# Kernel optimization log

Measured on AMD Instinct MI355X. Metric: run time of the kernel, lower is better.

## Reference

```python
import jax, jax.numpy as jnp
import numpy as np

T, N, E = 48, 1000, 32000
D_IN, H = 32, 64


def setup_inputs() -> dict:
    key = jax.random.key(0)
    ks = jax.random.split(key, 14)
    p = lambda k, s: (jax.random.normal(k, s, dtype=jnp.float32) * 0.05)
    return {
        "x": jax.random.normal(ks[0], (T, N, D_IN), dtype=jnp.float32),
        "edge_index": jax.random.randint(ks[1], (2, E), 0, N, dtype=jnp.int32),
        "hidden_state": jnp.zeros((N, H), jnp.float32),
        "cell_state": jnp.zeros((N, H), jnp.float32),
        # GCNConv 1 (lin weight stored as [in, out] so x @ W matches x @ lin.weight.T)
        "Wg1": p(ks[2], (D_IN, H)), "bg1": p(ks[3], (H,)),
        # GCNConv 2
        "Wg2": p(ks[4], (H, H)), "bg2": p(ks[5], (H,)),
        # LSTMCell params, torch gate order (i, f, g, o)
        "W_ih": p(ks[6], (4 * H, H)), "W_hh": p(ks[7], (4 * H, H)),
        "b_ih": p(ks[8], (4 * H,)), "b_hh": p(ks[9], (4 * H,)),
        # final Linear(hidden_dim * num_nodes -> num_nodes)
        "W_lin": p(ks[10], (N, H * N)), "b_lin": p(ks[11], (N,)),
    }


def _gcn_norm(edge_index, num_nodes):
    """PyG GCNConv default: add self loops, symmetric D^-1/2 (A+I) D^-1/2 norm."""
    loops = jnp.arange(num_nodes, dtype=edge_index.dtype)
    src = jnp.concatenate([edge_index[0], loops])
    dst = jnp.concatenate([edge_index[1], loops])
    deg = jax.ops.segment_sum(jnp.ones(src.shape[0], jnp.float32), dst,
                              num_segments=num_nodes)
    dinv = jax.lax.rsqrt(jnp.maximum(deg, 1.0))  # self loops guarantee deg >= 1
    norm = dinv[src] * dinv[dst]
    return src, dst, norm


def _gcn(x, W, b, src, dst, norm, num_nodes):
    x = x @ W                              # [N, out]
    msg = x[src] * norm[:, None]           # gather + scale  [E+N, out]
    return jax.ops.segment_sum(msg, dst, num_segments=num_nodes) + b


def reference(x, edge_index, hidden_state, cell_state,
              Wg1, bg1, Wg2, bg2, W_ih, W_hh, b_ih, b_hh, W_lin, b_lin):
    src, dst, norm = _gcn_norm(edge_index, N)

    def step(carry, xt):
        h, c = carry
        g = jax.nn.relu(_gcn(xt, Wg1, bg1, src, dst, norm, N))
        g = _gcn(g, Wg2, bg2, src, dst, norm, N)
        gates = g @ W_ih.T + b_ih + h @ W_hh.T + b_hh   # [N, 4H]
        i, f, gg, o = jnp.split(gates, 4, axis=-1)
        c = jax.nn.sigmoid(f) * c + jax.nn.sigmoid(i) * jnp.tanh(gg)
        h = jax.nn.sigmoid(o) * jnp.tanh(c)
        return (h, c), h

    (hidden_state, cell_state), h_seq = jax.lax.scan(step, (hidden_state, cell_state), x)
    flat = h_seq.reshape(T, N * H)                      # view(-1, hidden*num_nodes)
    out = flat @ W_lin.T + b_lin                        # [T, N]
    out = out.reshape(-1, N, 4)                         # [T/4, N, 4]
    return out, hidden_state, cell_state
```

## Files before the change

kernel.cpp:

```cpp
#include <hip/hip_runtime.h>
#include <math.h>

#define T_STEPS 48
#define N_NODES 1000
#define E_EDGES 32000
#define DIN     32
#define H_DIM   64

#define O_INDEG  0
#define O_FILL   1024
#define O_ROWPTR 2048
#define O_CSRC   4096
#define O_CNORM  36864
#define O_DINV   69632
#define O_SELF   70656
#define O_BUF0   71680
#define O_BUF1   (71680 + 3072000)

typedef __attribute__((ext_vector_type(8))) short short8;
typedef __attribute__((ext_vector_type(4))) float f32x4;

__device__ __forceinline__ float sigmf(float v) { return 1.0f / (1.0f + __expf(-v)); }

__global__ void k_zero(int* __restrict__ p) { p[blockIdx.x * 256 + threadIdx.x] = 0; }

__global__ void k_count(const int* __restrict__ ei, int* __restrict__ indeg) {
  int e = blockIdx.x * 256 + threadIdx.x;
  if (e < E_EDGES) atomicAdd(&indeg[ei[E_EDGES + e]], 1);
}

__global__ void k_scan(const int* __restrict__ indeg, int* __restrict__ rowptr,
                       float* __restrict__ dinv, float* __restrict__ selfn) {
  __shared__ int sdat[1024];
  int tid = threadIdx.x;
  int v = (tid < N_NODES) ? indeg[tid] : 0;
  sdat[tid] = v;
  __syncthreads();
  for (int off = 1; off < 1024; off <<= 1) {
    int add = (tid >= off) ? sdat[tid - off] : 0;
    __syncthreads();
    sdat[tid] += add;
    __syncthreads();
  }
  if (tid < N_NODES) {
    rowptr[tid + 1] = sdat[tid];
    float di = rsqrtf((float)(v + 1));
    dinv[tid] = di;
    selfn[tid] = di * di;
  }
  if (tid == 0) rowptr[0] = 0;
}

__global__ void k_scatter(const int* __restrict__ ei, const int* __restrict__ rowptr,
                          int* __restrict__ fill, const float* __restrict__ dinv,
                          int* __restrict__ csrc, float* __restrict__ cnorm) {
  int e = blockIdx.x * 256 + threadIdx.x;
  if (e >= E_EDGES) return;
  int s = ei[e], d = ei[E_EDGES + e];
  int pos = atomicAdd(&fill[d], 1);
  int idx = rowptr[d] + pos;
  csrc[idx] = s;
  cnorm[idx] = dinv[s] * dinv[d];
}

__global__ void __launch_bounds__(256) k_t1(const float* __restrict__ x,
                                            const float* __restrict__ Wg1,
                                            float* __restrict__ T1) {
  __shared__ float sWT[H_DIM * 36];
  __shared__ float sx[4][DIN];
  const int tid = threadIdx.x, wv = tid >> 6, h = tid & 63;
  for (int i = tid; i < DIN * H_DIM; i += 256) sWT[(i & 63) * 36 + (i >> 6)] = Wg1[i];
  __syncthreads();
  const int r0 = blockIdx.x * 64 + wv * 16;
  const float4* wrow = (const float4*)&sWT[h * 36];
  for (int it = 0; it < 16; ++it) {
    const int r = r0 + it;
    if (h < DIN) sx[wv][h] = x[r * DIN + h];
    float acc = 0.f;
    const float4* xp = (const float4*)&sx[wv][0];
#pragma unroll
    for (int k4 = 0; k4 < 8; ++k4) {
      float4 xv = xp[k4], wv4 = wrow[k4];
      acc += xv.x * wv4.x + xv.y * wv4.y + xv.z * wv4.z + xv.w * wv4.w;
    }
    T1[r * H_DIM + h] = acc;
  }
}

__device__ __forceinline__ float gath_node(const float* __restrict__ Tsrc,
                                           const int* __restrict__ es,
                                           const float* __restrict__ ew,
                                           int cnt, int h) {
  float a0 = 0.f, a1 = 0.f, a2 = 0.f, a3 = 0.f;
  float a4 = 0.f, a5 = 0.f, a6 = 0.f, a7 = 0.f;
  int e = 0;
  if (cnt >= 8) {
    float p0 = Tsrc[es[0] * 64 + h], p1 = Tsrc[es[1] * 64 + h];
    float p2 = Tsrc[es[2] * 64 + h], p3 = Tsrc[es[3] * 64 + h];
    float p4 = Tsrc[es[4] * 64 + h], p5 = Tsrc[es[5] * 64 + h];
    float p6 = Tsrc[es[6] * 64 + h], p7 = Tsrc[es[7] * 64 + h];
    for (e = 8; e + 8 <= cnt; e += 8) {
      float n0 = Tsrc[es[e + 0] * 64 + h], n1 = Tsrc[es[e + 1] * 64 + h];
      float n2 = Tsrc[es[e + 2] * 64 + h], n3 = Tsrc[es[e + 3] * 64 + h];
      float n4 = Tsrc[es[e + 4] * 64 + h], n5 = Tsrc[es[e + 5] * 64 + h];
      float n6 = Tsrc[es[e + 6] * 64 + h], n7 = Tsrc[es[e + 7] * 64 + h];
      a0 += ew[e - 8] * p0; a1 += ew[e - 7] * p1;
      a2 += ew[e - 6] * p2; a3 += ew[e - 5] * p3;
      a4 += ew[e - 4] * p4; a5 += ew[e - 3] * p5;
      a6 += ew[e - 2] * p6; a7 += ew[e - 1] * p7;
      p0 = n0; p1 = n1; p2 = n2; p3 = n3; p4 = n4; p5 = n5; p6 = n6; p7 = n7;
    }
    a0 += ew[e - 8] * p0; a1 += ew[e - 7] * p1;
    a2 += ew[e - 6] * p2; a3 += ew[e - 5] * p3;
    a4 += ew[e - 4] * p4; a5 += ew[e - 3] * p5;
    a6 += ew[e - 2] * p6; a7 += ew[e - 1] * p7;
  }
  for (; e < cnt; ++e) a0 += ew[e] * Tsrc[es[e] * 64 + h];
  return ((a0 + a1) + (a2 + a3)) + ((a4 + a5) + (a6 + a7));
}

#define ECHUNK 768
__global__ void __launch_bounds__(256) k_gath(const float* __restrict__ Tall,
                                              const float* __restrict__ bias,
                                              const int* __restrict__ rowptr,
                                              const int* __restrict__ csrc,
                                              const float* __restrict__ cnorm,
                                              const float* __restrict__ selfn,
                                              float* __restrict__ Dall, int relu) {
  __shared__ int   s_src[ECHUNK];
  __shared__ float s_wt[ECHUNK];
  __shared__ float sb[64];
  const int tid = threadIdx.x, wv = tid >> 6, h = tid & 63;
  if (tid < 64) sb[tid] = bias[tid];
  const int t = blockIdx.x >> 6, nb16 = (blockIdx.x & 63) * 16;
  if (nb16 >= N_NODES) return;
  const float* Tsrc = Tall + t * 64000;
  float* dst = Dall + t * 64000;
  const int nE = (nb16 + 16 < N_NODES) ? nb16 + 16 : N_NODES;
  const int r0 = rowptr[nb16], r1 = rowptr[nE];
  const int tot = r1 - r0;
  const bool fits = (tot <= ECHUNK);
  if (fits)
    for (int i = tid; i < tot; i += 256) { s_src[i] = csrc[r0 + i]; s_wt[i] = cnorm[r0 + i]; }
  __syncthreads();
  for (int i = 0; i < 4; ++i) {
    const int n = nb16 + wv * 4 + i;
    if (n >= N_NODES) continue;
    const int a = rowptr[n], b = rowptr[n + 1];
    float acc = selfn[n] * Tsrc[n * 64 + h];
    if (fits) {
      acc += gath_node(Tsrc, s_src + (a - r0), s_wt + (a - r0), b - a, h);
    } else {
      for (int e = a; e < b; ++e) acc += cnorm[e] * Tsrc[csrc[e] * 64 + h];
    }
    acc += sb[h];
    if (relu) acc = fmaxf(acc, 0.f);
    dst[n * 64 + h] = acc;
  }
}

__global__ void __launch_bounds__(256) k_mm2(const float* __restrict__ G1,
                                             const float* __restrict__ Wg2,
                                             float* __restrict__ T2) {
  __shared__ float sW[H_DIM * H_DIM];
  __shared__ float sx[4][H_DIM];
  const int tid = threadIdx.x, wv = tid >> 6, h = tid & 63;
  for (int i = tid; i < H_DIM * H_DIM; i += 256) sW[i] = Wg2[i];
  __syncthreads();
  const int r0 = blockIdx.x * 64 + wv * 16;
  for (int it = 0; it < 16; ++it) {
    const int r = r0 + it;
    sx[wv][h] = G1[r * 64 + h];
    float acc = 0.f;
#pragma unroll
    for (int k = 0; k < H_DIM; ++k) acc += sx[wv][k] * sW[k * H_DIM + h];
    T2[r * 64 + h] = acc;
  }
}

__global__ void __launch_bounds__(256) k_lstm(const float* __restrict__ G2,
                                              const float* __restrict__ h0,
                                              const float* __restrict__ c0,
                                              const float* __restrict__ Wih,
                                              const float* __restrict__ Whh,
                                              const float* __restrict__ bih,
                                              const float* __restrict__ bhh,
                                              float* __restrict__ hsg,
                                              float* __restrict__ outp) {
  const int tid = threadIdx.x, nb = blockIdx.x;
  __shared__ float sh[64];
  __shared__ float sg2[2][64];
  __shared__ float sgates[256];
  float4 Wih4[16], Whh4[16];
  {
    const float4* wp = (const float4*)(Wih + tid * H_DIM);
    const float4* vp = (const float4*)(Whh + tid * H_DIM);
#pragma unroll
    for (int k = 0; k < 16; ++k) { Wih4[k] = wp[k]; Whh4[k] = vp[k]; }
  }
  const float bsum = bih[tid] + bhh[tid];
  float creg = 0.f;
  if (tid < 64) {
    sh[tid] = h0[nb * 64 + tid];
    creg = c0[nb * 64 + tid];
    sg2[0][tid] = G2[nb * 64 + tid];
  }
  __syncthreads();
  for (int t = 0; t < T_STEPS; ++t) {
    const int cur = t & 1;
    float gnext = 0.f;
    if (t < T_STEPS - 1 && tid < 64) gnext = G2[(t + 1) * 64000 + nb * 64 + tid];
    float gv = bsum;
    const float4* gp = (const float4*)&sg2[cur][0];
    const float4* hp = (const float4*)sh;
#pragma unroll
    for (int k = 0; k < 16; ++k) {
      float4 a = gp[k], b = hp[k];
      gv += a.x * Wih4[k].x + a.y * Wih4[k].y + a.z * Wih4[k].z + a.w * Wih4[k].w;
      gv += b.x * Whh4[k].x + b.y * Whh4[k].y + b.z * Whh4[k].z + b.w * Whh4[k].w;
    }
    sgates[tid] = gv;
    __syncthreads();
    if (tid < 64) {
      float iv = sgates[tid], fv = sgates[64 + tid], gg = sgates[128 + tid], ov = sgates[192 + tid];
      float cn = sigmf(fv) * creg + sigmf(iv) * tanhf(gg);
      float hn = sigmf(ov) * tanhf(cn);
      creg = cn;
      sh[tid] = hn;
      hsg[t * 64000 + nb * 64 + tid] = hn;
      if (t < T_STEPS - 1) sg2[cur ^ 1][tid] = gnext;
    }
    __syncthreads();
  }
  if (tid < 64) {
    outp[48000 + nb * 64 + tid] = sh[tid];
    outp[48000 + 64000 + nb * 64 + tid] = creg;
  }
}

__global__ void k_cvt(const float* __restrict__ src, unsigned* __restrict__ dst) {
  const int id = blockIdx.x * 256 + threadIdx.x;
  const float4 v = ((const float4*)src)[id];
  unsigned lo, hi;
  asm("v_cvt_pk_bf16_f32 %0, %1, %2" : "=v"(lo) : "v"(v.x), "v"(v.y));
  asm("v_cvt_pk_bf16_f32 %0, %1, %2" : "=v"(hi) : "v"(v.z), "v"(v.w));
  ((uint2*)dst)[id] = make_uint2(lo, hi);
}

__global__ void __launch_bounds__(256) k_gemmM(const unsigned short* __restrict__ hsb,
                                               const float* __restrict__ Wlin,
                                               float* __restrict__ part) {
  const int tid = threadIdx.x;
  const int kc = blockIdx.x & 15, nt = blockIdx.x >> 4;
  const int wv = tid >> 6, l = tid & 63;
  const int lr = l & 15, kg = l >> 4;
  const int kcbase = kc * 4000;
  const int kp = kc * 4 + wv;

  const unsigned short* ap0 = hsb + (size_t)(0  + lr) * 64000 + kcbase + kg * 8 + wv * 32;
  const unsigned short* ap1 = hsb + (size_t)(16 + lr) * 64000 + kcbase + kg * 8 + wv * 32;
  const unsigned short* ap2 = hsb + (size_t)(32 + lr) * 64000 + kcbase + kg * 8 + wv * 32;
  int nrow = nt * 16 + lr; if (nrow > N_NODES - 1) nrow = N_NODES - 1;
  const float* bp = Wlin + (size_t)nrow * 64000 + kcbase + kg * 8 + wv * 32;

  f32x4 acc0 = {0.f, 0.f, 0.f, 0.f}, acc1 = acc0, acc2 = acc0;

  for (int s = wv; s < 125; s += 4) {
    const short8 a0 = *(const short8*)ap0;
    const short8 a1 = *(const short8*)ap1;
    const short8 a2 = *(const short8*)ap2;
    const float4 b0 = *(const float4*)bp;
    const float4 b1 = *(const float4*)(bp + 4);
    unsigned p0, p1, p2, p3;
    asm("v_cvt_pk_bf16_f32 %0, %1, %2" : "=v"(p0) : "v"(b0.x), "v"(b0.y));
    asm("v_cvt_pk_bf16_f32 %0, %1, %2" : "=v"(p1) : "v"(b0.z), "v"(b0.w));
    asm("v_cvt_pk_bf16_f32 %0, %1, %2" : "=v"(p2) : "v"(b1.x), "v"(b1.y));
    asm("v_cvt_pk_bf16_f32 %0, %1, %2" : "=v"(p3) : "v"(b1.z), "v"(b1.w));
    union { unsigned u[4]; short8 s; } bu;
    bu.u[0] = p0; bu.u[1] = p1; bu.u[2] = p2; bu.u[3] = p3;
    acc0 = __builtin_amdgcn_mfma_f32_16x16x32_bf16(a0, bu.s, acc0, 0, 0, 0);
    acc1 = __builtin_amdgcn_mfma_f32_16x16x32_bf16(a1, bu.s, acc1, 0, 0, 0);
    acc2 = __builtin_amdgcn_mfma_f32_16x16x32_bf16(a2, bu.s, acc2, 0, 0, 0);
    ap0 += 128; ap1 += 128; ap2 += 128; bp += 128;
  }

  const int n = nt * 16 + lr;
  if (n < N_NODES) {
    const int trow = kg * 4;
    float* base = part + (size_t)(kp * 48) * 1000 + n;
#pragma unroll
    for (int j = 0; j < 4; ++j) base[(0  + trow + j) * 1000] = acc0[j];
#pragma unroll
    for (int j = 0; j < 4; ++j) base[(16 + trow + j) * 1000] = acc1[j];
#pragma unroll
    for (int j = 0; j < 4; ++j) base[(32 + trow + j) * 1000] = acc2[j];
  }
}

__global__ void k_reduce(const float* __restrict__ part, const float* __restrict__ blin,
                         float* __restrict__ outp) {
  const int id = blockIdx.x * 256 + threadIdx.x;
  if (id >= T_STEPS * N_NODES) return;
  const int t = id / N_NODES, n = id - t * N_NODES;
  float s = blin[n];
#pragma unroll 8
  for (int kp = 0; kp < 64; ++kp) s += part[(size_t)(kp * 48 + t) * 1000 + n];
  outp[id] = s;
}

extern "C" void kernel_launch(void* const* d_in, const int* in_sizes, int n_in,
                              void* d_out, int out_size, void* d_ws, size_t ws_size,
                              hipStream_t stream) {
  const float* x    = (const float*)d_in[0];
  const int*   ei   = (const int*)d_in[1];
  const float* h0   = (const float*)d_in[2];
  const float* c0   = (const float*)d_in[3];
  const float* Wg1  = (const float*)d_in[4];
  const float* bg1  = (const float*)d_in[5];
  const float* Wg2  = (const float*)d_in[6];
  const float* bg2  = (const float*)d_in[7];
  const float* Wih  = (const float*)d_in[8];
  const float* Whh  = (const float*)d_in[9];
  const float* bih  = (const float*)d_in[10];
  const float* bhh  = (const float*)d_in[11];
  const float* Wlin = (const float*)d_in[12];
  const float* blin = (const float*)d_in[13];
  float* outp = (float*)d_out;
  float* wsf  = (float*)d_ws;
  int*   wsi  = (int*)d_ws;

  int*   indeg  = wsi + O_INDEG;
  int*   fill   = wsi + O_FILL;
  int*   rowptr = wsi + O_ROWPTR;
  int*   csrc   = wsi + O_CSRC;
  float* cnorm  = wsf + O_CNORM;
  float* dinv   = wsf + O_DINV;
  float* selfn  = wsf + O_SELF;
  float* buf0   = wsf + O_BUF0;
  float* buf1   = wsf + O_BUF1;

  k_zero<<<8, 256, 0, stream>>>(wsi);
  k_count<<<(E_EDGES + 255) / 256, 256, 0, stream>>>(ei, indeg);
  k_scan<<<1, 1024, 0, stream>>>(indeg, rowptr, dinv, selfn);
  k_scatter<<<(E_EDGES + 255) / 256, 256, 0, stream>>>(ei, rowptr, fill, dinv, csrc, cnorm);

  k_t1<<<750, 256, 0, stream>>>(x, Wg1, buf0);
  k_gath<<<3072, 256, 0, stream>>>(buf0, bg1, rowptr, csrc, cnorm, selfn, buf1, 1);
  k_mm2<<<750, 256, 0, stream>>>(buf1, Wg2, buf0);
  k_gath<<<3072, 256, 0, stream>>>(buf0, bg2, rowptr, csrc, cnorm, selfn, buf1, 0);
  k_lstm<<<1000, 256, 0, stream>>>(buf1, h0, c0, Wih, Whh, bih, bhh, buf0, outp);

  k_cvt<<<3000, 256, 0, stream>>>(buf0, (unsigned*)buf1);
  k_gemmM<<<16 * 63, 256, 0, stream>>>((const unsigned short*)buf1, Wlin, buf0);
  k_reduce<<<(T_STEPS * N_NODES + 255) / 256, 256, 0, stream>>>(buf0, blin, outp);
}
```

Baseline: 356.3 us.

## Vectorize GCN gather, fuse bf16 conversion into LSTM, prefetch GEMM operands

The gather kernel now splits each node's edges across four lane groups, with each lane loading a float4 of features, and combines the partial sums with cross-lane shuffles. When the workspace is large enough, the LSTM kernel writes hidden states directly as rounded bf16. This removes the separate conversion kernel and one fp32 round trip through memory. The final MFMA GEMM loop also software-prefetches the next A/B fragments to overlap loads with compute. The costs are extra registers and a code path that depends on workspace size.

New measurement: 366.7 us. +2.9%, slower.

```diff
diff --git a/kernel.cpp b/kernel.cpp
--- a/kernel.cpp
+++ b/kernel.cpp
@@ -16,9 +16,12 @@
 #define O_SELF   70656
 #define O_BUF0   71680
 #define O_BUF1   (71680 + 3072000)
+#define O_HSB    (71680 + 6144000)
+#define WS_NEED_HSB ((size_t)(O_HSB + 1536000) * 4)
 
 typedef __attribute__((ext_vector_type(8))) short short8;
 typedef __attribute__((ext_vector_type(4))) float f32x4;
+typedef __attribute__((ext_vector_type(4))) unsigned int uint32x4;
 
 __device__ __forceinline__ float sigmf(float v) { return 1.0f / (1.0f + __expf(-v)); }
 
@@ -87,38 +90,6 @@
   }
 }
 
-__device__ __forceinline__ float gath_node(const float* __restrict__ Tsrc,
-                                           const int* __restrict__ es,
-                                           const float* __restrict__ ew,
-                                           int cnt, int h) {
-  float a0 = 0.f, a1 = 0.f, a2 = 0.f, a3 = 0.f;
-  float a4 = 0.f, a5 = 0.f, a6 = 0.f, a7 = 0.f;
-  int e = 0;
-  if (cnt >= 8) {
-    float p0 = Tsrc[es[0] * 64 + h], p1 = Tsrc[es[1] * 64 + h];
-    float p2 = Tsrc[es[2] * 64 + h], p3 = Tsrc[es[3] * 64 + h];
-    float p4 = Tsrc[es[4] * 64 + h], p5 = Tsrc[es[5] * 64 + h];
-    float p6 = Tsrc[es[6] * 64 + h], p7 = Tsrc[es[7] * 64 + h];
-    for (e = 8; e + 8 <= cnt; e += 8) {
-      float n0 = Tsrc[es[e + 0] * 64 + h], n1 = Tsrc[es[e + 1] * 64 + h];
-      float n2 = Tsrc[es[e + 2] * 64 + h], n3 = Tsrc[es[e + 3] * 64 + h];
-      float n4 = Tsrc[es[e + 4] * 64 + h], n5 = Tsrc[es[e + 5] * 64 + h];
-      float n6 = Tsrc[es[e + 6] * 64 + h], n7 = Tsrc[es[e + 7] * 64 + h];
-      a0 += ew[e - 8] * p0; a1 += ew[e - 7] * p1;
-      a2 += ew[e - 6] * p2; a3 += ew[e - 5] * p3;
-      a4 += ew[e - 4] * p4; a5 += ew[e - 3] * p5;
-      a6 += ew[e - 2] * p6; a7 += ew[e - 1] * p7;
-      p0 = n0; p1 = n1; p2 = n2; p3 = n3; p4 = n4; p5 = n5; p6 = n6; p7 = n7;
-    }
-    a0 += ew[e - 8] * p0; a1 += ew[e - 7] * p1;
-    a2 += ew[e - 6] * p2; a3 += ew[e - 5] * p3;
-    a4 += ew[e - 4] * p4; a5 += ew[e - 3] * p5;
-    a6 += ew[e - 2] * p6; a7 += ew[e - 1] * p7;
-  }
-  for (; e < cnt; ++e) a0 += ew[e] * Tsrc[es[e] * 64 + h];
-  return ((a0 + a1) + (a2 + a3)) + ((a4 + a5) + (a6 + a7));
-}
-
 #define ECHUNK 768
 __global__ void __launch_bounds__(256) k_gath(const float* __restrict__ Tall,
                                               const float* __restrict__ bias,
@@ -129,9 +100,8 @@
                                               float* __restrict__ Dall, int relu) {
   __shared__ int   s_src[ECHUNK];
   __shared__ float s_wt[ECHUNK];
-  __shared__ float sb[64];
-  const int tid = threadIdx.x, wv = tid >> 6, h = tid & 63;
-  if (tid < 64) sb[tid] = bias[tid];
+  const int tid = threadIdx.x, wv = tid >> 6, lane = tid & 63;
+  const int h4 = lane & 15, eq = lane >> 4;
   const int t = blockIdx.x >> 6, nb16 = (blockIdx.x & 63) * 16;
   if (nb16 >= N_NODES) return;
   const float* Tsrc = Tall + t * 64000;
@@ -146,16 +116,58 @@
   for (int i = 0; i < 4; ++i) {
     const int n = nb16 + wv * 4 + i;
     if (n >= N_NODES) continue;
-    const int a = rowptr[n], b = rowptr[n + 1];
-    float acc = selfn[n] * Tsrc[n * 64 + h];
+    const int a = rowptr[n] - r0;
+    const int cnt = rowptr[n] - r0 >= 0 ? rowptr[n + 1] - rowptr[n] : 0;
+    float4 acc = make_float4(0.f, 0.f, 0.f, 0.f);
+    if (eq == 0) {
+      const float4 sv = *(const float4*)&Tsrc[n * 64 + h4 * 4];
+      const float sw = selfn[n];
+      acc.x = sw * sv.x; acc.y = sw * sv.y; acc.z = sw * sv.z; acc.w = sw * sv.w;
+    }
     if (fits) {
-      acc += gath_node(Tsrc, s_src + (a - r0), s_wt + (a - r0), b - a, h);
+      int e = a + eq;
+      const int end = a + cnt;
+      float4 pv = make_float4(0.f, 0.f, 0.f, 0.f);
+      float pw = 0.f;
+      bool have = (e < end);
+      if (have) {
+        const int s = s_src[e]; pw = s_wt[e];
+        pv = *(const float4*)&Tsrc[s * 64 + h4 * 4];
+      }
+      e += 4;
+      while (__any(have)) {
+        float4 nv = make_float4(0.f, 0.f, 0.f, 0.f);
+        float nw = 0.f;
+        const bool hnx = (e < end);
+        if (hnx) {
+          const int s2 = s_src[e]; nw = s_wt[e];
+          nv = *(const float4*)&Tsrc[s2 * 64 + h4 * 4];
+        }
+        acc.x += pw * pv.x; acc.y += pw * pv.y; acc.z += pw * pv.z; acc.w += pw * pv.w;
+        pv = nv; pw = nw; have = hnx; e += 4;
+      }
     } else {
-      for (int e = a; e < b; ++e) acc += cnorm[e] * Tsrc[csrc[e] * 64 + h];
-    }
-    acc += sb[h];
-    if (relu) acc = fmaxf(acc, 0.f);
-    dst[n * 64 + h] = acc;
+      const int A = rowptr[n], B = rowptr[n + 1];
+      for (int e2 = A + eq; e2 < B; e2 += 4) {
+        const int s = csrc[e2];
+        const float w = cnorm[e2];
+        const float4 v = *(const float4*)&Tsrc[s * 64 + h4 * 4];
+        acc.x += w * v.x; acc.y += w * v.y; acc.z += w * v.z; acc.w += w * v.w;
+      }
+    }
+    acc.x += __shfl_xor(acc.x, 16, 64); acc.y += __shfl_xor(acc.y, 16, 64);
+    acc.z += __shfl_xor(acc.z, 16, 64); acc.w += __shfl_xor(acc.w, 16, 64);
+    acc.x += __shfl_xor(acc.x, 32, 64); acc.y += __shfl_xor(acc.y, 32, 64);
+    acc.z += __shfl_xor(acc.z, 32, 64); acc.w += __shfl_xor(acc.w, 32, 64);
+    if (eq == 0) {
+      const float4 b4 = *(const float4*)&bias[h4 * 4];
+      float4 o = make_float4(acc.x + b4.x, acc.y + b4.y, acc.z + b4.z, acc.w + b4.w);
+      if (relu) {
+        o.x = fmaxf(o.x, 0.f); o.y = fmaxf(o.y, 0.f);
+        o.z = fmaxf(o.z, 0.f); o.w = fmaxf(o.w, 0.f);
+      }
+      *(float4*)&dst[n * 64 + h4 * 4] = o;
+    }
   }
 }
 
@@ -186,6 +198,7 @@
                                               const float* __restrict__ bih,
                                               const float* __restrict__ bhh,
                                               float* __restrict__ hsg,
+                                              unsigned short* __restrict__ hsb,
                                               float* __restrict__ outp) {
   const int tid = threadIdx.x, nb = blockIdx.x;
   __shared__ float sh[64];
@@ -227,7 +240,13 @@
       float hn = sigmf(ov) * tanhf(cn);
       creg = cn;
       sh[tid] = hn;
-      hsg[t * 64000 + nb * 64 + tid] = hn;
+      if (hsb) {
+        unsigned u = __float_as_uint(hn);
+        u += 0x7fff + ((u >> 16) & 1);
+        hsb[t * 64000 + nb * 64 + tid] = (unsigned short)(u >> 16);
+      } else {
+        hsg[t * 64000 + nb * 64 + tid] = hn;
+      }
       if (t < T_STEPS - 1) sg2[cur ^ 1][tid] = gnext;
     }
     __syncthreads();
@@ -265,23 +284,33 @@
 
   f32x4 acc0 = {0.f, 0.f, 0.f, 0.f}, acc1 = acc0, acc2 = acc0;
 
+  short8 a0c = *(const short8*)ap0;
+  short8 a1c = *(const short8*)ap1;
+  short8 a2c = *(const short8*)ap2;
+  float4 b0c = *(const float4*)bp;
+  float4 b1c = *(const float4*)(bp + 4);
+
   for (int s = wv; s < 125; s += 4) {
-    const short8 a0 = *(const short8*)ap0;
-    const short8 a1 = *(const short8*)ap1;
-    const short8 a2 = *(const short8*)ap2;
-    const float4 b0 = *(const float4*)bp;
-    const float4 b1 = *(const float4*)(bp + 4);
+    short8 a0n, a1n, a2n; float4 b0n, b1n;
+    if (s + 4 < 125) {
+      ap0 += 128; ap1 += 128; ap2 += 128; bp += 128;
+      a0n = *(const short8*)ap0;
+      a1n = *(const short8*)ap1;
+      a2n = *(const short8*)ap2;
+      b0n = *(const float4*)bp;
+      b1n = *(const float4*)(bp + 4);
+    }
     unsigned p0, p1, p2, p3;
-    asm("v_cvt_pk_bf16_f32 %0, %1, %2" : "=v"(p0) : "v"(b0.x), "v"(b0.y));
-    asm("v_cvt_pk_bf16_f32 %0, %1, %2" : "=v"(p1) : "v"(b0.z), "v"(b0.w));
-    asm("v_cvt_pk_bf16_f32 %0, %1, %2" : "=v"(p2) : "v"(b1.x), "v"(b1.y));
-    asm("v_cvt_pk_bf16_f32 %0, %1, %2" : "=v"(p3) : "v"(b1.z), "v"(b1.w));
-    union { unsigned u[4]; short8 s; } bu;
-    bu.u[0] = p0; bu.u[1] = p1; bu.u[2] = p2; bu.u[3] = p3;
-    acc0 = __builtin_amdgcn_mfma_f32_16x16x32_bf16(a0, bu.s, acc0, 0, 0, 0);
-    acc1 = __builtin_amdgcn_mfma_f32_16x16x32_bf16(a1, bu.s, acc1, 0, 0, 0);
-    acc2 = __builtin_amdgcn_mfma_f32_16x16x32_bf16(a2, bu.s, acc2, 0, 0, 0);
-    ap0 += 128; ap1 += 128; ap2 += 128; bp += 128;
+    asm("v_cvt_pk_bf16_f32 %0, %1, %2" : "=v"(p0) : "v"(b0c.x), "v"(b0c.y));
+    asm("v_cvt_pk_bf16_f32 %0, %1, %2" : "=v"(p1) : "v"(b0c.z), "v"(b0c.w));
+    asm("v_cvt_pk_bf16_f32 %0, %1, %2" : "=v"(p2) : "v"(b1c.x), "v"(b1c.y));
+    asm("v_cvt_pk_bf16_f32 %0, %1, %2" : "=v"(p3) : "v"(b1c.z), "v"(b1c.w));
+    uint32x4 bu = {p0, p1, p2, p3};
+    const short8 bs = __builtin_bit_cast(short8, bu);
+    acc0 = __builtin_amdgcn_mfma_f32_16x16x32_bf16(a0c, bs, acc0, 0, 0, 0);
+    acc1 = __builtin_amdgcn_mfma_f32_16x16x32_bf16(a1c, bs, acc1, 0, 0, 0);
+    acc2 = __builtin_amdgcn_mfma_f32_16x16x32_bf16(a2c, bs, acc2, 0, 0, 0);
+    a0c = a0n; a1c = a1n; a2c = a2n; b0c = b0n; b1c = b1n;
   }
 
   const int n = nt * 16 + lr;
@@ -339,6 +368,8 @@
   float* buf0   = wsf + O_BUF0;
   float* buf1   = wsf + O_BUF1;
 
+  const bool big = ws_size >= WS_NEED_HSB;
+
   k_zero<<<8, 256, 0, stream>>>(wsi);
   k_count<<<(E_EDGES + 255) / 256, 256, 0, stream>>>(ei, indeg);
   k_scan<<<1, 1024, 0, stream>>>(indeg, rowptr, dinv, selfn);
@@ -348,9 +379,18 @@
   k_gath<<<3072, 256, 0, stream>>>(buf0, bg1, rowptr, csrc, cnorm, selfn, buf1, 1);
   k_mm2<<<750, 256, 0, stream>>>(buf1, Wg2, buf0);
   k_gath<<<3072, 256, 0, stream>>>(buf0, bg2, rowptr, csrc, cnorm, selfn, buf1, 0);
-  k_lstm<<<1000, 256, 0, stream>>>(buf1, h0, c0, Wih, Whh, bih, bhh, buf0, outp);
-
-  k_cvt<<<3000, 256, 0, stream>>>(buf0, (unsigned*)buf1);
-  k_gemmM<<<16 * 63, 256, 0, stream>>>((const unsigned short*)buf1, Wlin, buf0);
+
+  unsigned short* hsb;
+  if (big) {
+    hsb = (unsigned short*)(wsf + O_HSB);
+    k_lstm<<<1000, 256, 0, stream>>>(buf1, h0, c0, Wih, Whh, bih, bhh,
+                                     buf0, hsb, outp);
+  } else {
+    k_lstm<<<1000, 256, 0, stream>>>(buf1, h0, c0, Wih, Whh, bih, bhh,
+                                     buf0, (unsigned short*)nullptr, outp);
+    k_cvt<<<3000, 256, 0, stream>>>(buf0, (unsigned*)buf1);
+    hsb = (unsigned short*)buf1;
+  }
+  k_gemmM<<<16 * 63, 256, 0, stream>>>(hsb, Wlin, buf0);
   k_reduce<<<(T_STEPS * N_NODES + 255) / 256, 256, 0, stream>>>(buf0, blin, outp);
 }
```

## Fuse bf16 hidden-state conversion into LSTM and pipeline final GEMM through LDS

Applied to the files above, without the earlier changes.

The LSTM kernel now writes its hidden states directly as bf16 into a new workspace region, which removes the separate conversion kernel. The final linear layer gets a new GEMM kernel that triple-buffers hidden-state and W_lin tiles in LDS using async global_load_lds with swizzled addressing. The K split changes from 64 to 100 partials. This path is chosen only when the workspace is large enough, and it adds more partial sums for the reduce kernel to read.

Measured after the change: 368.9 us. 3.5% more time.

```diff
diff --git a/kernel.cpp b/kernel.cpp
--- a/kernel.cpp
+++ b/kernel.cpp
@@ -16,11 +16,19 @@
 #define O_SELF   70656
 #define O_BUF0   71680
 #define O_BUF1   (71680 + 3072000)
+#define O_HSB    (71680 + 6144000)
+#define WS_NEED_HSB ((size_t)(O_HSB + 1536000) * 4)
 
 typedef __attribute__((ext_vector_type(8))) short short8;
 typedef __attribute__((ext_vector_type(4))) float f32x4;
+typedef __attribute__((ext_vector_type(4))) unsigned int uint32x4;
 
 __device__ __forceinline__ float sigmf(float v) { return 1.0f / (1.0f + __expf(-v)); }
+
+__device__ __forceinline__ void gld16(const void* g, void* l) {
+  __builtin_amdgcn_global_load_lds((const __attribute__((address_space(1))) void*)g,
+                                   (__attribute__((address_space(3))) void*)l, 16, 0, 0);
+}
 
 __global__ void k_zero(int* __restrict__ p) { p[blockIdx.x * 256 + threadIdx.x] = 0; }
 
@@ -186,6 +194,7 @@
                                               const float* __restrict__ bih,
                                               const float* __restrict__ bhh,
                                               float* __restrict__ hsg,
+                                              unsigned short* __restrict__ hsb,
                                               float* __restrict__ outp) {
   const int tid = threadIdx.x, nb = blockIdx.x;
   __shared__ float sh[64];
@@ -227,7 +236,13 @@
       float hn = sigmf(ov) * tanhf(cn);
       creg = cn;
       sh[tid] = hn;
-      hsg[t * 64000 + nb * 64 + tid] = hn;
+      if (hsb) {
+        unsigned u = __float_as_uint(hn);
+        u += 0x7fff + ((u >> 16) & 1);
+        hsb[t * 64000 + nb * 64 + tid] = (unsigned short)(u >> 16);
+      } else {
+        hsg[t * 64000 + nb * 64 + tid] = hn;
+      }
       if (t < T_STEPS - 1) sg2[cur ^ 1][tid] = gnext;
     }
     __syncthreads();
@@ -245,6 +260,104 @@
   asm("v_cvt_pk_bf16_f32 %0, %1, %2" : "=v"(lo) : "v"(v.x), "v"(v.y));
   asm("v_cvt_pk_bf16_f32 %0, %1, %2" : "=v"(hi) : "v"(v.z), "v"(v.w));
   ((uint2*)dst)[id] = make_uint2(lo, hi);
+}
+
+#define G16_KC   25
+#define G16_KR   2560
+#define G16_NCH  20
+#define G16_AF   3072
+#define G16_BF   5120
+
+__global__ void __launch_bounds__(256) k_gemm16(const unsigned short* __restrict__ hsb,
+                                                const float* __restrict__ Wlin,
+                                                float* __restrict__ part) {
+  __shared__ float lds[3 * G16_BF];
+  const int tid = threadIdx.x;
+  const int kc = blockIdx.x % G16_KC, nt = blockIdx.x / G16_KC;
+  const int nbase = nt * 16;
+  const int kbase = kc * G16_KR;
+  const int wv = tid >> 6, l = tid & 63;
+  const int lr = l & 15, kg = l >> 4;
+  const int kp = kc * 4 + wv;
+
+#define STAGE16(c)                                                              \
+  {                                                                             \
+    char* db = (char*)(lds + ((c) % 3) * G16_BF);                               \
+    const int bk = kbase + (c) * 128;                                           \
+    _Pragma("unroll")                                                           \
+    for (int r = 0; r < 3; ++r) {                                               \
+      const int q = r * 256 + tid;                                              \
+      const int row = q >> 4, pos = q & 15;                                     \
+      gld16(hsb + (size_t)row * 64000 + bk + (((pos - row) & 15) * 8),          \
+            db + q * 16);                                                       \
+    }                                                                           \
+    _Pragma("unroll")                                                           \
+    for (int r = 0; r < 2; ++r) {                                               \
+      const int q = r * 256 + tid;                                              \
+      const int row = q >> 5, pos = q & 31;                                     \
+      int ngl = nbase + row; if (ngl > N_NODES - 1) ngl = N_NODES - 1;          \
+      gld16(Wlin + (size_t)ngl * 64000 + bk + (((pos - row) & 31) * 4),         \
+            db + 12288 + q * 16);                                               \
+    }                                                                           \
+  }
+
+  f32x4 acc0 = {0.f, 0.f, 0.f, 0.f}, acc1 = acc0, acc2 = acc0;
+  const int apos = (wv * 4 + kg + lr) & 15;
+  const int g0 = wv * 8 + kg * 2;
+
+  STAGE16(0);
+  STAGE16(1);
+
+  for (int c = 0; c < G16_NCH; ++c) {
+    if (c + 2 < G16_NCH) {
+      STAGE16(c + 2);
+      __builtin_amdgcn_sched_barrier(0);
+      asm volatile("s_waitcnt vmcnt(10)" ::: "memory");
+    } else if (c + 1 < G16_NCH) {
+      asm volatile("s_waitcnt vmcnt(5)" ::: "memory");
+    } else {
+      asm volatile("s_waitcnt vmcnt(0)" ::: "memory");
+    }
+    __builtin_amdgcn_sched_barrier(0);
+    __builtin_amdgcn_s_barrier();
+    __builtin_amdgcn_sched_barrier(0);
+    {
+      const float* db = lds + (c % 3) * G16_BF;
+      const short8* Ab = (const short8*)db;
+      const float4* Wb = (const float4*)(db + G16_AF);
+      const short8 a0 = Ab[(0  + lr) * 16 + apos];
+      const short8 a1 = Ab[(16 + lr) * 16 + apos];
+      const short8 a2 = Ab[(32 + lr) * 16 + apos];
+      const float4 w0 = Wb[lr * 32 + ((g0 + lr) & 31)];
+      const float4 w1 = Wb[lr * 32 + ((g0 + 1 + lr) & 31)];
+      unsigned p0, p1, p2, p3;
+      asm("v_cvt_pk_bf16_f32 %0, %1, %2" : "=v"(p0) : "v"(w0.x), "v"(w0.y));
+      asm("v_cvt_pk_bf16_f32 %0, %1, %2" : "=v"(p1) : "v"(w0.z), "v"(w0.w));
+      asm("v_cvt_pk_bf16_f32 %0, %1, %2" : "=v"(p2) : "v"(w1.x), "v"(w1.y));
+      asm("v_cvt_pk_bf16_f32 %0, %1, %2" : "=v"(p3) : "v"(w1.z), "v"(w1.w));
+      uint32x4 bu = {p0, p1, p2, p3};
+      const short8 bs = __builtin_bit_cast(short8, bu);
+      acc0 = __builtin_amdgcn_mfma_f32_16x16x32_bf16(a0, bs, acc0, 0, 0, 0);
+      acc1 = __builtin_amdgcn_mfma_f32_16x16x32_bf16(a1, bs, acc1, 0, 0, 0);
+      acc2 = __builtin_amdgcn_mfma_f32_16x16x32_bf16(a2, bs, acc2, 0, 0, 0);
+    }
+    __builtin_amdgcn_sched_barrier(0);
+    __builtin_amdgcn_s_barrier();
+    __builtin_amdgcn_sched_barrier(0);
+  }
+#undef STAGE16
+
+  const int n = nbase + lr;
+  if (n < N_NODES) {
+    const int trow = kg * 4;
+    float* base = part + (size_t)(kp * 48) * 1000 + n;
+#pragma unroll
+    for (int j = 0; j < 4; ++j) base[(0  + trow + j) * 1000] = acc0[j];
+#pragma unroll
+    for (int j = 0; j < 4; ++j) base[(16 + trow + j) * 1000] = acc1[j];
+#pragma unroll
+    for (int j = 0; j < 4; ++j) base[(32 + trow + j) * 1000] = acc2[j];
+  }
 }
 
 __global__ void __launch_bounds__(256) k_gemmM(const unsigned short* __restrict__ hsb,
@@ -276,11 +389,11 @@
     asm("v_cvt_pk_bf16_f32 %0, %1, %2" : "=v"(p1) : "v"(b0.z), "v"(b0.w));
     asm("v_cvt_pk_bf16_f32 %0, %1, %2" : "=v"(p2) : "v"(b1.x), "v"(b1.y));
     asm("v_cvt_pk_bf16_f32 %0, %1, %2" : "=v"(p3) : "v"(b1.z), "v"(b1.w));
-    union { unsigned u[4]; short8 s; } bu;
-    bu.u[0] = p0; bu.u[1] = p1; bu.u[2] = p2; bu.u[3] = p3;
-    acc0 = __builtin_amdgcn_mfma_f32_16x16x32_bf16(a0, bu.s, acc0, 0, 0, 0);
-    acc1 = __builtin_amdgcn_mfma_f32_16x16x32_bf16(a1, bu.s, acc1, 0, 0, 0);
-    acc2 = __builtin_amdgcn_mfma_f32_16x16x32_bf16(a2, bu.s, acc2, 0, 0, 0);
+    uint32x4 bu = {p0, p1, p2, p3};
+    const short8 bs = __builtin_bit_cast(short8, bu);
+    acc0 = __builtin_amdgcn_mfma_f32_16x16x32_bf16(a0, bs, acc0, 0, 0, 0);
+    acc1 = __builtin_amdgcn_mfma_f32_16x16x32_bf16(a1, bs, acc1, 0, 0, 0);
+    acc2 = __builtin_amdgcn_mfma_f32_16x16x32_bf16(a2, bs, acc2, 0, 0, 0);
     ap0 += 128; ap1 += 128; ap2 += 128; bp += 128;
   }
 
@@ -298,13 +411,12 @@
 }
 
 __global__ void k_reduce(const float* __restrict__ part, const float* __restrict__ blin,
-                         float* __restrict__ outp) {
+                         float* __restrict__ outp, int np) {
   const int id = blockIdx.x * 256 + threadIdx.x;
   if (id >= T_STEPS * N_NODES) return;
   const int t = id / N_NODES, n = id - t * N_NODES;
   float s = blin[n];
-#pragma unroll 8
-  for (int kp = 0; kp < 64; ++kp) s += part[(size_t)(kp * 48 + t) * 1000 + n];
+  for (int kp = 0; kp < np; ++kp) s += part[(size_t)(kp * 48 + t) * 1000 + n];
   outp[id] = s;
 }
 
@@ -339,6 +451,8 @@
   float* buf0   = wsf + O_BUF0;
   float* buf1   = wsf + O_BUF1;
 
+  const bool big = ws_size >= WS_NEED_HSB;
+
   k_zero<<<8, 256, 0, stream>>>(wsi);
   k_count<<<(E_EDGES + 255) / 256, 256, 0, stream>>>(ei, indeg);
   k_scan<<<1, 1024, 0, stream>>>(indeg, rowptr, dinv, selfn);
@@ -348,9 +462,18 @@
   k_gath<<<3072, 256, 0, stream>>>(buf0, bg1, rowptr, csrc, cnorm, selfn, buf1, 1);
   k_mm2<<<750, 256, 0, stream>>>(buf1, Wg2, buf0);
   k_gath<<<3072, 256, 0, stream>>>(buf0, bg2, rowptr, csrc, cnorm, selfn, buf1, 0);
-  k_lstm<<<1000, 256, 0, stream>>>(buf1, h0, c0, Wih, Whh, bih, bhh, buf0, outp);
-
-  k_cvt<<<3000, 256, 0, stream>>>(buf0, (unsigned*)buf1);
-  k_gemmM<<<16 * 63, 256, 0, stream>>>((const unsigned short*)buf1, Wlin, buf0);
-  k_reduce<<<(T_STEPS * N_NODES + 255) / 256, 256, 0, stream>>>(buf0, blin, outp);
-}
+
+  if (big) {
+    unsigned short* hsb = (unsigned short*)(wsf + O_HSB);
+    k_lstm<<<1000, 256, 0, stream>>>(buf1, h0, c0, Wih, Whh, bih, bhh,
+                                     buf0, hsb, outp);
+    k_gemm16<<<G16_KC * 63, 256, 0, stream>>>(hsb, Wlin, buf0);
+    k_reduce<<<(T_STEPS * N_NODES + 255) / 256, 256, 0, stream>>>(buf0, blin, outp, 100);
+  } else {
+    k_lstm<<<1000, 256, 0, stream>>>(buf1, h0, c0, Wih, Whh, bih, bhh,
+                                     buf0, (unsigned short*)nullptr, outp);
+    k_cvt<<<3000, 256, 0, stream>>>(buf0, (unsigned*)buf1);
+    k_gemmM<<<16 * 63, 256, 0, stream>>>((const unsigned short*)buf1, Wlin, buf0);
+    k_reduce<<<(T_STEPS * N_NODES + 255) / 256, 256, 0, stream>>>(buf0, blin, outp, 64);
+  }
+}
```

## Write bf16 hidden states from LSTM and reduce split-K partials in-block

Applied to the files above, without the earlier changes.

The LSTM kernel now writes its hidden states straight to a bf16 buffer, which removes the separate fp32-to-bf16 conversion kernel and the fp32 round trip through memory. A new GEMM kernel splits K into 40 chunks and sums the four waves' partials in shared memory, so the final reduction reads 40 partial planes instead of 64. The new path runs only if the workspace is large enough for the extra bf16 buffer, with the old path kept as a fallback. The cost is more blocks and shared-memory traffic per block in the GEMM.

Result: no change. 358.8 us (+0.7%).

```diff
diff --git a/kernel.cpp b/kernel.cpp
--- a/kernel.cpp
+++ b/kernel.cpp
@@ -16,9 +16,12 @@
 #define O_SELF   70656
 #define O_BUF0   71680
 #define O_BUF1   (71680 + 3072000)
+#define O_HSB    (71680 + 6144000)
+#define WS_NEED_HSB ((size_t)(O_HSB + 1536000) * 4)
 
 typedef __attribute__((ext_vector_type(8))) short short8;
 typedef __attribute__((ext_vector_type(4))) float f32x4;
+typedef __attribute__((ext_vector_type(4))) unsigned int uint32x4;
 
 __device__ __forceinline__ float sigmf(float v) { return 1.0f / (1.0f + __expf(-v)); }
 
@@ -186,6 +189,7 @@
                                               const float* __restrict__ bih,
                                               const float* __restrict__ bhh,
                                               float* __restrict__ hsg,
+                                              unsigned short* __restrict__ hsb,
                                               float* __restrict__ outp) {
   const int tid = threadIdx.x, nb = blockIdx.x;
   __shared__ float sh[64];
@@ -227,7 +231,13 @@
       float hn = sigmf(ov) * tanhf(cn);
       creg = cn;
       sh[tid] = hn;
-      hsg[t * 64000 + nb * 64 + tid] = hn;
+      if (hsb) {
+        unsigned u = __float_as_uint(hn);
+        u += 0x7fff + ((u >> 16) & 1);
+        hsb[t * 64000 + nb * 64 + tid] = (unsigned short)(u >> 16);
+      } else {
+        hsg[t * 64000 + nb * 64 + tid] = hn;
+      }
       if (t < T_STEPS - 1) sg2[cur ^ 1][tid] = gnext;
     }
     __syncthreads();
@@ -245,6 +255,67 @@
   asm("v_cvt_pk_bf16_f32 %0, %1, %2" : "=v"(lo) : "v"(v.x), "v"(v.y));
   asm("v_cvt_pk_bf16_f32 %0, %1, %2" : "=v"(hi) : "v"(v.z), "v"(v.w));
   ((uint2*)dst)[id] = make_uint2(lo, hi);
+}
+
+#define GS_KC 40
+__global__ void __launch_bounds__(256) k_gemmS(const unsigned short* __restrict__ hsb,
+                                               const float* __restrict__ Wlin,
+                                               float* __restrict__ part) {
+  __shared__ float4 red[4][3][64];
+  const int tid = threadIdx.x;
+  const int kc = blockIdx.x % GS_KC, nt = blockIdx.x / GS_KC;
+  const int wv = tid >> 6, l = tid & 63;
+  const int lr = l & 15, kg = l >> 4;
+  const int kcbase = kc * 1600;
+
+  const unsigned short* ap0 = hsb + (size_t)(0  + lr) * 64000 + kcbase + kg * 8 + wv * 32;
+  const unsigned short* ap1 = hsb + (size_t)(16 + lr) * 64000 + kcbase + kg * 8 + wv * 32;
+  const unsigned short* ap2 = hsb + (size_t)(32 + lr) * 64000 + kcbase + kg * 8 + wv * 32;
+  int nrow = nt * 16 + lr; if (nrow > N_NODES - 1) nrow = N_NODES - 1;
+  const float* bp = Wlin + (size_t)nrow * 64000 + kcbase + kg * 8 + wv * 32;
+
+  f32x4 acc0 = {0.f, 0.f, 0.f, 0.f}, acc1 = acc0, acc2 = acc0;
+
+  for (int s = wv; s < 50; s += 4) {
+    const short8 a0 = *(const short8*)ap0;
+    const short8 a1 = *(const short8*)ap1;
+    const short8 a2 = *(const short8*)ap2;
+    const float4 b0 = *(const float4*)bp;
+    const float4 b1 = *(const float4*)(bp + 4);
+    unsigned p0, p1, p2, p3;
+    asm("v_cvt_pk_bf16_f32 %0, %1, %2" : "=v"(p0) : "v"(b0.x), "v"(b0.y));
+    asm("v_cvt_pk_bf16_f32 %0, %1, %2" : "=v"(p1) : "v"(b0.z), "v"(b0.w));
+    asm("v_cvt_pk_bf16_f32 %0, %1, %2" : "=v"(p2) : "v"(b1.x), "v"(b1.y));
+    asm("v_cvt_pk_bf16_f32 %0, %1, %2" : "=v"(p3) : "v"(b1.z), "v"(b1.w));
+    uint32x4 bu = {p0, p1, p2, p3};
+    const short8 bs = __builtin_bit_cast(short8, bu);
+    acc0 = __builtin_amdgcn_mfma_f32_16x16x32_bf16(a0, bs, acc0, 0, 0, 0);
+    acc1 = __builtin_amdgcn_mfma_f32_16x16x32_bf16(a1, bs, acc1, 0, 0, 0);
+    acc2 = __builtin_amdgcn_mfma_f32_16x16x32_bf16(a2, bs, acc2, 0, 0, 0);
+    ap0 += 128; ap1 += 128; ap2 += 128; bp += 128;
+  }
+
+  red[wv][0][l] = make_float4(acc0[0], acc0[1], acc0[2], acc0[3]);
+  red[wv][1][l] = make_float4(acc1[0], acc1[1], acc1[2], acc1[3]);
+  red[wv][2][l] = make_float4(acc2[0], acc2[1], acc2[2], acc2[3]);
+  __syncthreads();
+  if (wv < 3) {
+    const float4 r0 = red[0][wv][l], r1 = red[1][wv][l];
+    const float4 r2 = red[2][wv][l], r3 = red[3][wv][l];
+    const float4 s4 = make_float4(r0.x + r1.x + r2.x + r3.x,
+                                  r0.y + r1.y + r2.y + r3.y,
+                                  r0.z + r1.z + r2.z + r3.z,
+                                  r0.w + r1.w + r2.w + r3.w);
+    const int n = nt * 16 + lr;
+    if (n < N_NODES) {
+      const int trow = wv * 16 + kg * 4;
+      float* base = part + (size_t)(kc * 48 + trow) * 1000 + n;
+      base[0]    = s4.x;
+      base[1000] = s4.y;
+      base[2000] = s4.z;
+      base[3000] = s4.w;
+    }
+  }
 }
 
 __global__ void __launch_bounds__(256) k_gemmM(const unsigned short* __restrict__ hsb,
@@ -276,11 +347,11 @@
     asm("v_cvt_pk_bf16_f32 %0, %1, %2" : "=v"(p1) : "v"(b0.z), "v"(b0.w));
     asm("v_cvt_pk_bf16_f32 %0, %1, %2" : "=v"(p2) : "v"(b1.x), "v"(b1.y));
     asm("v_cvt_pk_bf16_f32 %0, %1, %2" : "=v"(p3) : "v"(b1.z), "v"(b1.w));
-    union { unsigned u[4]; short8 s; } bu;
-    bu.u[0] = p0; bu.u[1] = p1; bu.u[2] = p2; bu.u[3] = p3;
-    acc0 = __builtin_amdgcn_mfma_f32_16x16x32_bf16(a0, bu.s, acc0, 0, 0, 0);
-    acc1 = __builtin_amdgcn_mfma_f32_16x16x32_bf16(a1, bu.s, acc1, 0, 0, 0);
-    acc2 = __builtin_amdgcn_mfma_f32_16x16x32_bf16(a2, bu.s, acc2, 0, 0, 0);
+    uint32x4 bu = {p0, p1, p2, p3};
+    const short8 bs = __builtin_bit_cast(short8, bu);
+    acc0 = __builtin_amdgcn_mfma_f32_16x16x32_bf16(a0, bs, acc0, 0, 0, 0);
+    acc1 = __builtin_amdgcn_mfma_f32_16x16x32_bf16(a1, bs, acc1, 0, 0, 0);
+    acc2 = __builtin_amdgcn_mfma_f32_16x16x32_bf16(a2, bs, acc2, 0, 0, 0);
     ap0 += 128; ap1 += 128; ap2 += 128; bp += 128;
   }
 
@@ -298,13 +369,12 @@
 }
 
 __global__ void k_reduce(const float* __restrict__ part, const float* __restrict__ blin,
-                         float* __restrict__ outp) {
+                         float* __restrict__ outp, int np) {
   const int id = blockIdx.x * 256 + threadIdx.x;
   if (id >= T_STEPS * N_NODES) return;
   const int t = id / N_NODES, n = id - t * N_NODES;
   float s = blin[n];
-#pragma unroll 8
-  for (int kp = 0; kp < 64; ++kp) s += part[(size_t)(kp * 48 + t) * 1000 + n];
+  for (int kp = 0; kp < np; ++kp) s += part[(size_t)(kp * 48 + t) * 1000 + n];
   outp[id] = s;
 }
 
@@ -339,6 +409,8 @@
   float* buf0   = wsf + O_BUF0;
   float* buf1   = wsf + O_BUF1;
 
+  const bool big = ws_size >= WS_NEED_HSB;
+
   k_zero<<<8, 256, 0, stream>>>(wsi);
   k_count<<<(E_EDGES + 255) / 256, 256, 0, stream>>>(ei, indeg);
   k_scan<<<1, 1024, 0, stream>>>(indeg, rowptr, dinv, selfn);
@@ -348,9 +420,18 @@
   k_gath<<<3072, 256, 0, stream>>>(buf0, bg1, rowptr, csrc, cnorm, selfn, buf1, 1);
   k_mm2<<<750, 256, 0, stream>>>(buf1, Wg2, buf0);
   k_gath<<<3072, 256, 0, stream>>>(buf0, bg2, rowptr, csrc, cnorm, selfn, buf1, 0);
-  k_lstm<<<1000, 256, 0, stream>>>(buf1, h0, c0, Wih, Whh, bih, bhh, buf0, outp);
-
-  k_cvt<<<3000, 256, 0, stream>>>(buf0, (unsigned*)buf1);
-  k_gemmM<<<16 * 63, 256, 0, stream>>>((const unsigned short*)buf1, Wlin, buf0);
-  k_reduce<<<(T_STEPS * N_NODES + 255) / 256, 256, 0, stream>>>(buf0, blin, outp);
-}
+
+  if (big) {
+    unsigned short* hsb = (unsigned short*)(wsf + O_HSB);
+    k_lstm<<<1000, 256, 0, stream>>>(buf1, h0, c0, Wih, Whh, bih, bhh,
+                                     buf0, hsb, outp);
+    k_gemmS<<<GS_KC * 63, 256, 0, stream>>>(hsb, Wlin, buf0);
+    k_reduce<<<(T_STEPS * N_NODES + 255) / 256, 256, 0, stream>>>(buf0, blin, outp, GS_KC);
+  } else {
+    k_lstm<<<1000, 256, 0, stream>>>(buf1, h0, c0, Wih, Whh, bih, bhh,
+                                     buf0, (unsigned short*)nullptr, outp);
+    k_cvt<<<3000, 256, 0, stream>>>(buf0, (unsigned*)buf1);
+    k_gemmM<<<16 * 63, 256, 0, stream>>>((const unsigned short*)buf1, Wlin, buf0);
+    k_reduce<<<(T_STEPS * N_NODES + 255) / 256, 256, 0, stream>>>(buf0, blin, outp, 64);
+  }
+}
```
